# Optimization experiments

Measured on AMD Instinct MI355X. Metric: run time of the kernel, lower is better.

The kernel has to match this reference:

```python
import jax, jax.numpy as jnp
import numpy as np

EPS = 1e-7  # tf.keras.backend.epsilon()
ROUTINGS = 3


def setup_inputs() -> dict:
    key = jax.random.key(0)
    k1, k2 = jax.random.split(key)
    x = jax.random.normal(k1, (64, 2048, 8), dtype=jnp.float32)
    W = jax.random.normal(k2, (32, 2048, 16, 8), dtype=jnp.float32) * 0.05
    return {"x": x, "W": W}


def _squash(s):
    # source squash: vectors / sqrt(sum(v^2) + eps)
    ssq = jnp.sum(s * s, axis=-1, keepdims=True)
    return s / jnp.sqrt(ssq + EPS)


def reference(x, W):
    # x: [B, N, I]; W: [J, N, D, I]
    # prediction vectors u_hat: [B, J, N, D]
    u_hat = jnp.einsum('bni,jndi->bjnd', x, W)
    b = jnp.zeros(u_hat.shape[:-1], dtype=u_hat.dtype)  # [B, J, N]
    v = None
    for i in range(ROUTINGS):
        c = jax.nn.softmax(b, axis=1)                       # coupling over output caps J
        s = jnp.einsum('bjnd,bjn->bjd', u_hat, c)           # weighted sum over input caps N
        v = _squash(s)                                      # [B, J, D]
        if i < ROUTINGS - 1:
            b = b + jnp.einsum('bjnd,bjd->bjn', u_hat, v)   # agreement update
    return v
```

## Files before the change

kernel.cpp:

```cpp
#include <hip/hip_runtime.h>


#define BB_ 64
#define NN_ 2048
#define II_ 8
#define JJ_ 32
#define DD_ 16
#define NCHUNKS 128
#define CHUNK 16
#define BG 8
#define NBG (BB_ / BG)
#define EPS_ 1e-7f

#define PARTIAL_FLOATS (NCHUNKS * BB_ * JJ_ * DD_)

typedef __attribute__((ext_vector_type(2))) float v2f;

template <int CTRL>
__device__ __forceinline__ float dpp_add(float v) {
  const int s = __builtin_amdgcn_update_dpp(
      0, __builtin_bit_cast(int, v), CTRL, 0xf, 0xf, true);
  return v + __builtin_bit_cast(float, s);
}
#define DPP_QP_XOR1 0xB1
#define DPP_QP_XOR2 0x4E
#define DPP_HALF_MIRROR 0x141
#define DPP_ROR8 0x128

template <int PHASE>
__global__ __launch_bounds__(256, 4) void caps_phase(
    const float* __restrict__ x, const float* __restrict__ W,
    const float* __restrict__ V, float* __restrict__ partial) {
  const int tid = threadIdx.x;
  const int j = tid >> 3;
  const int p = tid & 7;
  const int chunk = blockIdx.x & (NCHUNKS - 1);
  const int bg = blockIdx.x >> 7;
  const int b0 = bg * BG;
  const int n0 = chunk * CHUNK;

  __shared__ float lmat[BG][JJ_];
  __shared__ float cmat[BG][JJ_];

  float v0r[BG], v1r[BG];
  if (PHASE > 0) {
#pragma unroll
    for (int b = 0; b < BG; ++b) {
      const float2 vv =
          *(const float2*)&V[((size_t)(b0 + b) * JJ_ + j) * DD_ + 2 * p];
      v0r[b] = vv.x;
      v1r[b] = vv.y;
    }
  }

  v2f s[BG];
#pragma unroll
  for (int b = 0; b < BG; ++b) s[b] = (v2f)(0.f);

  const float* wp = W + (size_t)j * (NN_ * DD_ * II_) + (size_t)n0 * (DD_ * II_) +
                    (size_t)p * 16;
  float4 wc0 = ((const float4*)wp)[0];
  float4 wc1 = ((const float4*)wp)[1];
  float4 wc2 = ((const float4*)wp)[2];
  float4 wc3 = ((const float4*)wp)[3];

  for (int nl = 0; nl < CHUNK; ++nl) {
    const int n = n0 + nl;
    const int nn = (nl + 1 < CHUNK) ? nl + 1 : nl;
    const float4* np_ = (const float4*)(wp + (size_t)nn * (DD_ * II_));
    const float4 wn0 = np_[0], wn1 = np_[1], wn2 = np_[2], wn3 = np_[3];

    v2f wk0 = {wc0.x, wc2.x}, wk1 = {wc0.y, wc2.y};
    v2f wk2 = {wc0.z, wc2.z}, wk3 = {wc0.w, wc2.w};
    v2f wk4 = {wc1.x, wc3.x}, wk5 = {wc1.y, wc3.y};
    v2f wk6 = {wc1.z, wc3.z}, wk7 = {wc1.w, wc3.w};

    v2f u[BG];
#pragma unroll
    for (int b = 0; b < BG; ++b) {
      const float4* __restrict__ xr =
          (const float4*)(x + ((size_t)(b0 + b) * NN_ + n) * II_);
      const float4 xa = xr[0];
      const float4 xb = xr[1];
      v2f acc = wk0 * xa.x;
      acc += wk1 * xa.y;
      acc += wk2 * xa.z;
      acc += wk3 * xa.w;
      acc += wk4 * xb.x;
      acc += wk5 * xb.y;
      acc += wk6 * xb.z;
      acc += wk7 * xb.w;
      u[b] = acc;
    }

    if (PHASE == 0) {
#pragma unroll
      for (int b = 0; b < BG; ++b) s[b] += u[b];
    } else {
#pragma unroll
      for (int b = 0; b < BG; ++b) {
        float lp = u[b].x * v0r[b] + u[b].y * v1r[b];
        lp = dpp_add<DPP_QP_XOR1>(lp);
        lp = dpp_add<DPP_QP_XOR2>(lp);
        lp = dpp_add<DPP_HALF_MIRROR>(lp);
        if (p == 0) lmat[b][j] = lp;
      }
      __syncthreads();
      {
        const int jj = tid & 31;
        const int bb = tid >> 5;
        float e0 = __expf(lmat[bb][jj]);
        float m0 = e0;
        m0 = dpp_add<DPP_QP_XOR1>(m0);
        m0 = dpp_add<DPP_QP_XOR2>(m0);
        m0 = dpp_add<DPP_HALF_MIRROR>(m0);
        m0 = dpp_add<DPP_ROR8>(m0);
        m0 += __shfl_xor(m0, 16);
        cmat[bb][jj] = e0 * __builtin_amdgcn_rcpf(m0);
      }
      __syncthreads();
#pragma unroll
      for (int b = 0; b < BG; ++b) {
        const float c = cmat[b][j];
        s[b] += u[b] * c;
      }
    }

    wc0 = wn0;
    wc1 = wn1;
    wc2 = wn2;
    wc3 = wn3;
  }

  const float scale = (PHASE == 0) ? (1.0f / 32.0f) : 1.0f;
#pragma unroll
  for (int b = 0; b < BG; ++b) {
    const size_t off =
        ((size_t)chunk * BB_ + (b0 + b)) * (JJ_ * DD_) + j * DD_ + 2 * p;
    *(float2*)&partial[off] = make_float2(s[b].x * scale, s[b].y * scale);
  }
}

template <int MODE>
__global__ __launch_bounds__(128) void caps_reduce(
    const float* __restrict__ partial, float* __restrict__ V,
    float* __restrict__ out) {
  const int t = blockIdx.x * 128 + threadIdx.x;
  float s = 0.f;
#pragma unroll 8
  for (int c = 0; c < NCHUNKS; ++c)
    s += partial[(size_t)c * (BB_ * JJ_ * DD_) + t];
  float ss = s * s;
  ss += __shfl_xor(ss, 1);
  ss += __shfl_xor(ss, 2);
  ss += __shfl_xor(ss, 4);
  ss += __shfl_xor(ss, 8);
  const float v = s / sqrtf(ss + EPS_);
  if (MODE == 0)
    V[t] = v;
  else if (MODE == 1)
    V[t] += v;
  else
    out[t] = v;
}

extern "C" void kernel_launch(void* const* d_in, const int* in_sizes, int n_in,
                              void* d_out, int out_size, void* d_ws,
                              size_t ws_size, hipStream_t stream) {
  const float* x = (const float*)d_in[0];
  const float* W = (const float*)d_in[1];
  float* out = (float*)d_out;
  float* partial = (float*)d_ws;
  float* V = partial + PARTIAL_FLOATS;

  const dim3 kgrid(NBG * NCHUNKS);
  const dim3 rgrid((BB_ * JJ_ * DD_) / 128);

  caps_phase<0><<<kgrid, 256, 0, stream>>>(x, W, nullptr, partial);
  caps_reduce<0><<<rgrid, 128, 0, stream>>>(partial, V, out);
  caps_phase<1><<<kgrid, 256, 0, stream>>>(x, W, V, partial);
  caps_reduce<1><<<rgrid, 128, 0, stream>>>(partial, V, out);
  caps_phase<2><<<kgrid, 256, 0, stream>>>(x, W, V, partial);
  caps_reduce<2><<<rgrid, 128, 0, stream>>>(partial, V, out);
}
```

Before: 176.3 us.

## Double-buffer W prefetch and software-pipeline routing softmax across input capsules

Restructures the routing phase loop to process two input capsules per iteration with double-buffered LDS logit/coupling arrays, so the softmax for one capsule overlaps the u_hat computation and logit reduction of the next. This cuts the number of block barriers per capsule from two to one. W loads are now prefetched two steps ahead with two register sets, for both phase 0 and the routing phases. The cost is higher register pressure from keeping two u_hat sets and two W sets live, which could reduce occupancy under the launch bounds.

```diff
diff --git a/kernel.cpp b/kernel.cpp
--- a/kernel.cpp
+++ b/kernel.cpp
@@ -26,6 +26,68 @@
 #define DPP_QP_XOR2 0x4E
 #define DPP_HALF_MIRROR 0x141
 #define DPP_ROR8 0x128
+
+struct W8 {
+  v2f k[8];
+};
+
+__device__ __forceinline__ W8 loadW(const float* p) {
+  const float4* q = (const float4*)p;
+  const float4 t0 = q[0], t1 = q[1], t2 = q[2], t3 = q[3];
+  W8 w = {{{t0.x, t2.x}, {t0.y, t2.y},
+           {t0.z, t2.z}, {t0.w, t2.w},
+           {t1.x, t3.x}, {t1.y, t3.y},
+           {t1.z, t3.z}, {t1.w, t3.w}}};
+  return w;
+}
+
+__device__ __forceinline__ void compute_u(const W8& w, const float* __restrict__ x,
+                                          int b0, int n, v2f (&u)[BG]) {
+#pragma unroll
+  for (int b = 0; b < BG; ++b) {
+    const float4* __restrict__ xr =
+        (const float4*)(x + ((size_t)(b0 + b) * NN_ + n) * II_);
+    const float4 xa = xr[0];
+    const float4 xb = xr[1];
+    v2f acc = w.k[0] * xa.x;
+    acc += w.k[1] * xa.y;
+    acc += w.k[2] * xa.z;
+    acc += w.k[3] * xa.w;
+    acc += w.k[4] * xb.x;
+    acc += w.k[5] * xb.y;
+    acc += w.k[6] * xb.z;
+    acc += w.k[7] * xb.w;
+    u[b] = acc;
+  }
+}
+
+__device__ __forceinline__ void logits_to_lds(const v2f (&u)[BG],
+                                              const v2f (&vv)[BG],
+                                              float (*lrow)[JJ_], int j, int p) {
+#pragma unroll
+  for (int b = 0; b < BG; ++b) {
+    const v2f m = u[b] * vv[b];
+    float lp = m.x + m.y;
+    lp = dpp_add<DPP_QP_XOR1>(lp);
+    lp = dpp_add<DPP_QP_XOR2>(lp);
+    lp = dpp_add<DPP_HALF_MIRROR>(lp);
+    if (p == 0) lrow[b][j] = lp;
+  }
+}
+
+__device__ __forceinline__ void softmax_step(const float (*lrow)[JJ_],
+                                             float (*crow)[JJ_], int tid) {
+  const int jj = tid & 31;
+  const int bb = tid >> 5;
+  const float e0 = __expf(lrow[bb][jj]);
+  float m0 = e0;
+  m0 = dpp_add<DPP_QP_XOR1>(m0);
+  m0 = dpp_add<DPP_QP_XOR2>(m0);
+  m0 = dpp_add<DPP_HALF_MIRROR>(m0);
+  m0 = dpp_add<DPP_ROR8>(m0);
+  m0 += __shfl_xor(m0, 16);
+  crow[bb][jj] = e0 * __builtin_amdgcn_rcpf(m0);
+}
 
 template <int PHASE>
 __global__ __launch_bounds__(256, 4) void caps_phase(
@@ -39,97 +101,77 @@
   const int b0 = bg * BG;
   const int n0 = chunk * CHUNK;
 
-  __shared__ float lmat[BG][JJ_];
-  __shared__ float cmat[BG][JJ_];
-
-  float v0r[BG], v1r[BG];
-  if (PHASE > 0) {
+  const float* wp = W + (size_t)j * (NN_ * DD_ * II_) +
+                    (size_t)n0 * (DD_ * II_) + (size_t)p * 16;
+
+  v2f s[BG];
+#pragma unroll
+  for (int b = 0; b < BG; ++b) s[b] = (v2f)(0.f);
+
+  if (PHASE == 0) {
+    W8 wA = loadW(wp);
+    W8 wB = loadW(wp + 128);
+    for (int nl = 0; nl < CHUNK; nl += 2) {
+      v2f u[BG];
+      compute_u(wA, x, b0, n0 + nl, u);
+#pragma unroll
+      for (int b = 0; b < BG; ++b) s[b] += u[b];
+      {
+        const int nf = (nl + 2 < CHUNK) ? nl + 2 : CHUNK - 1;
+        wA = loadW(wp + (size_t)nf * 128);
+      }
+      compute_u(wB, x, b0, n0 + nl + 1, u);
+#pragma unroll
+      for (int b = 0; b < BG; ++b) s[b] += u[b];
+      {
+        const int nf = (nl + 3 < CHUNK) ? nl + 3 : CHUNK - 1;
+        wB = loadW(wp + (size_t)nf * 128);
+      }
+    }
+  } else {
+    __shared__ float lmat[2][BG][JJ_];
+    __shared__ float cmat[2][BG][JJ_];
+
+    v2f vv[BG];
 #pragma unroll
     for (int b = 0; b < BG; ++b) {
-      const float2 vv =
+      const float2 t =
           *(const float2*)&V[((size_t)(b0 + b) * JJ_ + j) * DD_ + 2 * p];
-      v0r[b] = vv.x;
-      v1r[b] = vv.y;
+      vv[b] = __builtin_bit_cast(v2f, t);
     }
-  }
-
-  v2f s[BG];
-#pragma unroll
-  for (int b = 0; b < BG; ++b) s[b] = (v2f)(0.f);
-
-  const float* wp = W + (size_t)j * (NN_ * DD_ * II_) + (size_t)n0 * (DD_ * II_) +
-                    (size_t)p * 16;
-  float4 wc0 = ((const float4*)wp)[0];
-  float4 wc1 = ((const float4*)wp)[1];
-  float4 wc2 = ((const float4*)wp)[2];
-  float4 wc3 = ((const float4*)wp)[3];
-
-  for (int nl = 0; nl < CHUNK; ++nl) {
-    const int n = n0 + nl;
-    const int nn = (nl + 1 < CHUNK) ? nl + 1 : nl;
-    const float4* np_ = (const float4*)(wp + (size_t)nn * (DD_ * II_));
-    const float4 wn0 = np_[0], wn1 = np_[1], wn2 = np_[2], wn3 = np_[3];
-
-    v2f wk0 = {wc0.x, wc2.x}, wk1 = {wc0.y, wc2.y};
-    v2f wk2 = {wc0.z, wc2.z}, wk3 = {wc0.w, wc2.w};
-    v2f wk4 = {wc1.x, wc3.x}, wk5 = {wc1.y, wc3.y};
-    v2f wk6 = {wc1.z, wc3.z}, wk7 = {wc1.w, wc3.w};
-
-    v2f u[BG];
-#pragma unroll
-    for (int b = 0; b < BG; ++b) {
-      const float4* __restrict__ xr =
-          (const float4*)(x + ((size_t)(b0 + b) * NN_ + n) * II_);
-      const float4 xa = xr[0];
-      const float4 xb = xr[1];
-      v2f acc = wk0 * xa.x;
-      acc += wk1 * xa.y;
-      acc += wk2 * xa.z;
-      acc += wk3 * xa.w;
-      acc += wk4 * xb.x;
-      acc += wk5 * xb.y;
-      acc += wk6 * xb.z;
-      acc += wk7 * xb.w;
-      u[b] = acc;
+
+    W8 wA = loadW(wp);
+    W8 wB = loadW(wp + 128);
+    v2f uA[BG], uB[BG];
+    compute_u(wA, x, b0, n0, uA);
+    logits_to_lds(uA, vv, lmat[0], j, p);
+    __syncthreads();
+
+    for (int nl = 0; nl < CHUNK; nl += 2) {
+      {
+        const int nf = (nl + 2 < CHUNK) ? nl + 2 : CHUNK - 1;
+        wA = loadW(wp + (size_t)nf * 128);
+      }
+      softmax_step(lmat[0], cmat[0], tid);
+      compute_u(wB, x, b0, n0 + nl + 1, uB);
+      logits_to_lds(uB, vv, lmat[1], j, p);
+      __syncthreads();
+#pragma unroll
+      for (int b = 0; b < BG; ++b) s[b] += uA[b] * cmat[0][b][j];
+
+      {
+        const int nf = (nl + 3 < CHUNK) ? nl + 3 : CHUNK - 1;
+        wB = loadW(wp + (size_t)nf * 128);
+      }
+      softmax_step(lmat[1], cmat[1], tid);
+      if (nl + 2 < CHUNK) {
+        compute_u(wA, x, b0, n0 + nl + 2, uA);
+        logits_to_lds(uA, vv, lmat[0], j, p);
+      }
+      __syncthreads();
+#pragma unroll
+      for (int b = 0; b < BG; ++b) s[b] += uB[b] * cmat[1][b][j];
     }
-
-    if (PHASE == 0) {
-#pragma unroll
-      for (int b = 0; b < BG; ++b) s[b] += u[b];
-    } else {
-#pragma unroll
-      for (int b = 0; b < BG; ++b) {
-        float lp = u[b].x * v0r[b] + u[b].y * v1r[b];
-        lp = dpp_add<DPP_QP_XOR1>(lp);
-        lp = dpp_add<DPP_QP_XOR2>(lp);
-        lp = dpp_add<DPP_HALF_MIRROR>(lp);
-        if (p == 0) lmat[b][j] = lp;
-      }
-      __syncthreads();
-      {
-        const int jj = tid & 31;
-        const int bb = tid >> 5;
-        float e0 = __expf(lmat[bb][jj]);
-        float m0 = e0;
-        m0 = dpp_add<DPP_QP_XOR1>(m0);
-        m0 = dpp_add<DPP_QP_XOR2>(m0);
-        m0 = dpp_add<DPP_HALF_MIRROR>(m0);
-        m0 = dpp_add<DPP_ROR8>(m0);
-        m0 += __shfl_xor(m0, 16);
-        cmat[bb][jj] = e0 * __builtin_amdgcn_rcpf(m0);
-      }
-      __syncthreads();
-#pragma unroll
-      for (int b = 0; b < BG; ++b) {
-        const float c = cmat[b][j];
-        s[b] += u[b] * c;
-      }
-    }
-
-    wc0 = wn0;
-    wc1 = wn1;
-    wc2 = wn2;
-    wc3 = wn3;
   }
 
   const float scale = (PHASE == 0) ? (1.0f / 32.0f) : 1.0f;
```

Result: slower. 183.7 us (+4.2%).
